# Performance work log

Measured on AMD Instinct MI355X. Metric: run time of the kernel, lower is better.

## Reference

```python
import jax, jax.numpy as jnp
import numpy as np

B, S, N, E = 8, 64, 512, 32  # batch, seq_size, node_num, embed_size


def setup_inputs() -> dict:
    key = jax.random.key(0)
    k0, k1, k2, k3, k4 = jax.random.split(key, 5)
    x = jax.random.normal(k0, (B, S, N), dtype=jnp.float32)
    # lin_w: Linear(2*S, E) -> weight (E, 2*S), bias (E,)
    W = jax.random.normal(k1, (E, 2 * S), dtype=jnp.float32) * (1.0 / np.sqrt(2 * S))
    b_w = jax.random.normal(k2, (E,), dtype=jnp.float32) * 0.01
    # lin_a: Linear(E, 1) -> weight (E,), bias scalar
    Wa = jax.random.normal(k3, (E,), dtype=jnp.float32) * (1.0 / np.sqrt(E))
    b_a = jax.random.normal(k4, (), dtype=jnp.float32) * 0.01
    return {"x": x, "W": W, "b_w": b_w, "Wa": Wa, "b_a": b_a}


def reference(x, W, b_w, Wa, b_a):
    # Faithful to MP_GAT.forward in eval mode (dropout = identity).
    # Algebraic decomposition: lin_w(cat(vi, vj)) = vi @ Wi^T + vj @ Wj^T + b,
    # where W = [Wi | Wj] along the input dim -- avoids the O(N^2 * 2S) concat.
    s = W.shape[1] // 2
    v = jnp.transpose(x, (0, 2, 1))          # (B, N, S)
    Wi, Wj = W[:, :s], W[:, s:]              # (E, S) each
    ti = jnp.einsum('bns,es->bne', v, Wi)    # (B, N, E)
    tj = jnp.einsum('bns,es->bne', v, Wj)    # (B, N, E)
    pre = ti[:, :, None, :] + tj[:, None, :, :] + b_w  # (B, N, N, E)
    xw = jnp.where(pre > 0, pre, 0.2 * pre)  # LeakyReLU(0.2)
    e = jnp.einsum('bije,e->bij', xw, Wa) + b_a        # (B, N, N) = lin_a(...).squeeze
    attention = jax.nn.softmax(e, axis=2)
    h = jax.nn.sigmoid(jnp.einsum('bij,bjs->bis', attention, v))  # (B, N, S)
    return jnp.transpose(h, (0, 2, 1)), attention      # (B, S, N), (B, N, N)
```

## Files before the change

### kernel.cpp

```cpp
#include <hip/hip_runtime.h>
#include <math.h>

#define BB 8
#define SS 64
#define NN 512
#define EE 32
#define IT 16

__device__ __forceinline__ unsigned short f2bf(float f) {
    union { float f; unsigned u; } v; v.f = f;
    unsigned r = v.u + 0x7fffu + ((v.u >> 16) & 1u);
    return (unsigned short)(r >> 16);
}
__device__ __forceinline__ float bflo(unsigned u) { return __uint_as_float(u << 16); }
__device__ __forceinline__ float bfhi(unsigned u) { return __uint_as_float(u & 0xffff0000u); }

__device__ __forceinline__ float qsum(float v) {
    v += __int_as_float(__builtin_amdgcn_mov_dpp(__float_as_int(v), 0xB1, 0xF, 0xF, true));
    v += __int_as_float(__builtin_amdgcn_mov_dpp(__float_as_int(v), 0x4E, 0xF, 0xF, true));
    return v;
}

__global__ __launch_bounds__(128) void proj_kernel(
    const float* __restrict__ x, const float* __restrict__ W,
    const float* __restrict__ b_w, const float* __restrict__ Wa,
    float* __restrict__ tip, unsigned short* __restrict__ tjb,
    float* __restrict__ cip, float* __restrict__ djp)
{
    __shared__ float sW[SS][65];
    const int t = threadIdx.x;
    const int wg = ((blockIdx.x & 7) << 6) | (blockIdx.x >> 3);
    const int b = wg >> 6;
    const int n0 = (wg & 63) << 3;

#pragma unroll
    for (int r = 0; r < 8; ++r) {
        int idx = r * 512 + t * 4;
        float4 w4 = *(const float4*)(W + idx);
        int e = idx >> 7;
        int sp = idx & 127;
        int eo = ((sp >> 6) << 5) | e;
        int s0 = sp & 63;
        sW[s0 + 0][eo] = w4.x;
        sW[s0 + 1][eo] = w4.y;
        sW[s0 + 2][eo] = w4.z;
        sW[s0 + 3][eo] = w4.w;
    }
    __syncthreads();

    const int eo = t & 63;
    const int ng = t >> 6;
    const float* xb = x + (size_t)b * SS * NN + n0 + (ng << 2);
    float a0 = 0.f, a1 = 0.f, a2 = 0.f, a3 = 0.f;
#pragma unroll 8
    for (int s = 0; s < SS; ++s) {
        float wv = sW[s][eo];
        float4 xv = *(const float4*)(xb + (size_t)s * NN);
        a0 = fmaf(wv, xv.x, a0);
        a1 = fmaf(wv, xv.y, a1);
        a2 = fmaf(wv, xv.z, a2);
        a3 = fmaf(wv, xv.w, a3);
    }
    const int e = eo & 31;
    const bool isI = eo < EE;
    if (isI) {
        float bias = b_w[e];
        a0 += bias; a1 += bias; a2 += bias; a3 += bias;
        *(float4*)(tip + ((size_t)(b * EE + e)) * NN + n0 + (ng << 2)) =
            make_float4(a0, a1, a2, a3);
    } else {
        unsigned u0 = f2bf(a0) | ((unsigned)f2bf(a1) << 16);
        unsigned u1 = f2bf(a2) | ((unsigned)f2bf(a3) << 16);
        *(uint2*)(tjb + ((size_t)(b * EE + e)) * NN + n0 + (ng << 2)) =
            make_uint2(u0, u1);
    }

    float wa = Wa[e];
    float r0 = wa * a0, r1 = wa * a1, r2 = wa * a2, r3 = wa * a3;
#pragma unroll
    for (int off = 1; off <= 16; off <<= 1) {
        r0 += __shfl_xor(r0, off);
        r1 += __shfl_xor(r1, off);
        r2 += __shfl_xor(r2, off);
        r3 += __shfl_xor(r3, off);
    }
    if (eo == 0)
        *(float4*)(cip + (size_t)b * NN + n0 + (ng << 2)) = make_float4(r0, r1, r2, r3);
    if (eo == 32)
        *(float4*)(djp + (size_t)b * NN + n0 + (ng << 2)) = make_float4(r0, r1, r2, r3);
}

__global__ __launch_bounds__(512, 2) void attn_kernel(
    const float* __restrict__ x,
    const float* __restrict__ tip,
    const unsigned short* __restrict__ tjb,
    const float* __restrict__ cip,
    const float* __restrict__ djp,
    const float* __restrict__ Wa,
    float* __restrict__ out0,
    float* __restrict__ out1)
{
    __shared__ __align__(16) unsigned short stj[EE * NN];
    __shared__ __align__(16) unsigned scT[NN * 12];
    __shared__ __align__(16) float s_tiT[IT][36];
    __shared__ __align__(16) float hp[8 * SS * 20];
    __shared__ __align__(16) float red[8][IT];
    __shared__ float s_inv[IT];

    const int t = threadIdx.x;
    const int wg = ((blockIdx.x & 7) << 5) | (blockIdx.x >> 3);
    const int b = wg >> 5;
    const int i0 = (wg & 31) << 4;
    const int lane = t & 63;
    const int w = t >> 6;

    {
        int i = t & 15, e = t >> 4;
        s_tiT[i][e] = tip[((size_t)(b * EE + e)) * NN + i0 + i];
    }
    {
        const uint4* src = (const uint4*)(tjb + (size_t)b * EE * NN);
        uint4* dst = (uint4*)stj;
#pragma unroll
        for (int r = 0; r < 4; ++r) dst[r * 512 + t] = src[r * 512 + t];
    }
    __syncthreads();

    const int ip = t & 7;
    const int jc = t >> 3;
    const int j0 = jc << 3;
    const int ia = 2 * ip, ib2 = 2 * ip + 1;

    float rti0[EE], rti1[EE];
#pragma unroll
    for (int q = 0; q < 8; ++q) {
        float4 v = *(const float4*)&s_tiT[ia][q << 2];
        rti0[4 * q + 0] = v.x; rti0[4 * q + 1] = v.y;
        rti0[4 * q + 2] = v.z; rti0[4 * q + 3] = v.w;
        float4 u = *(const float4*)&s_tiT[ib2][q << 2];
        rti1[4 * q + 0] = u.x; rti1[4 * q + 1] = u.y;
        rti1[4 * q + 2] = u.z; rti1[4 * q + 3] = u.w;
    }

    float acc0[8], acc1[8];
#pragma unroll
    for (int k = 0; k < 8; ++k) { acc0[k] = 0.f; acc1[k] = 0.f; }

#pragma unroll
    for (int e = 0; e < EE; ++e) {
        uint4 d = *(const uint4*)&stj[e * NN + j0];
        float wa = Wa[e];
        float t0 = rti0[e], t1 = rti1[e];
        float tjf[8];
        tjf[0] = bflo(d.x); tjf[1] = bfhi(d.x);
        tjf[2] = bflo(d.y); tjf[3] = bfhi(d.y);
        tjf[4] = bflo(d.z); tjf[5] = bfhi(d.z);
        tjf[6] = bflo(d.w); tjf[7] = bfhi(d.w);
#pragma unroll
        for (int k = 0; k < 8; ++k) {
            acc0[k] = fmaf(fabsf(t0 + tjf[k]), wa, acc0[k]);
            acc1[k] = fmaf(fabsf(t1 + tjf[k]), wa, acc1[k]);
        }
    }

    float dj8[8];
    {
        float4 d0 = *(const float4*)(djp + (size_t)b * NN + j0);
        float4 d1 = *(const float4*)(djp + (size_t)b * NN + j0 + 4);
        dj8[0] = d0.x; dj8[1] = d0.y; dj8[2] = d0.z; dj8[3] = d0.w;
        dj8[4] = d1.x; dj8[5] = d1.y; dj8[6] = d1.z; dj8[7] = d1.w;
    }
    float c0 = cip[(size_t)b * NN + i0 + ia];
    float c1 = cip[(size_t)b * NN + i0 + ib2];
    float pr0[8], pr1[8];
#pragma unroll
    for (int k = 0; k < 8; ++k) {
        pr0[k] = __expf(fmaf(0.4f, acc0[k], 0.6f * (c0 + dj8[k])));
        pr1[k] = __expf(fmaf(0.4f, acc1[k], 0.6f * (c1 + dj8[k])));
    }

#pragma unroll
    for (int k = 0; k < 8; ++k) {
        scT[(j0 + k) * 12 + ip] = f2bf(pr0[k]) | ((unsigned)f2bf(pr1[k]) << 16);
    }

    float rs0 = 0.f, rs1 = 0.f;
#pragma unroll
    for (int k = 0; k < 8; ++k) { rs0 += pr0[k]; rs1 += pr1[k]; }
#pragma unroll
    for (int off = 8; off <= 32; off <<= 1) {
        rs0 += __shfl_xor(rs0, off);
        rs1 += __shfl_xor(rs1, off);
    }
    if (lane < 8) { red[w][2 * lane] = rs0; red[w][2 * lane + 1] = rs1; }
    __syncthreads();
    if (t < IT) {
        float S = 0.f;
#pragma unroll
        for (int ww = 0; ww < 8; ++ww) S += red[ww][t];
        s_inv[t] = 1.0f / S;
    }
    __syncthreads();

    {
        float v0 = s_inv[ia], v1 = s_inv[ib2];
        float* r0p = out1 + ((size_t)(b * NN + i0 + ia)) * NN + j0;
        float* r1p = out1 + ((size_t)(b * NN + i0 + ib2)) * NN + j0;
        *(float4*)(r0p)     = make_float4(pr0[0]*v0, pr0[1]*v0, pr0[2]*v0, pr0[3]*v0);
        *(float4*)(r0p + 4) = make_float4(pr0[4]*v0, pr0[5]*v0, pr0[6]*v0, pr0[7]*v0);
        *(float4*)(r1p)     = make_float4(pr1[0]*v1, pr1[1]*v1, pr1[2]*v1, pr1[3]*v1);
        *(float4*)(r1p + 4) = make_float4(pr1[4]*v1, pr1[5]*v1, pr1[6]*v1, pr1[7]*v1);
    }

    const int jw = t & 3;
    const int sq = (t >> 2) & 7;
    const int ih = (t >> 5) & 1;
    const int w8 = t >> 6;
    float pacc[8][8];
#pragma unroll
    for (int r = 0; r < 8; ++r)
#pragma unroll
        for (int c = 0; c < 8; ++c) pacc[r][c] = 0.f;

    const float* xbb = x + (size_t)b * SS * NN;
#pragma unroll
    for (int uu = 0; uu < 4; ++uu) {
        const int jb = uu * 128 + w8 * 16 + jw * 4;
        float xq[8][4];
#pragma unroll
        for (int r = 0; r < 8; ++r) {
            float4 xv = *(const float4*)(xbb + (size_t)(sq + 8 * r) * NN + jb);
            xq[r][0] = xv.x; xq[r][1] = xv.y; xq[r][2] = xv.z; xq[r][3] = xv.w;
        }
#pragma unroll
        for (int v = 0; v < 4; ++v) {
            uint4 dd = *(const uint4*)&scT[(jb + v) * 12 + (ih << 2)];
            float ps[8];
            ps[0] = bflo(dd.x); ps[1] = bfhi(dd.x);
            ps[2] = bflo(dd.y); ps[3] = bfhi(dd.y);
            ps[4] = bflo(dd.z); ps[5] = bfhi(dd.z);
            ps[6] = bflo(dd.w); ps[7] = bfhi(dd.w);
#pragma unroll
            for (int r = 0; r < 8; ++r) {
                float xv = xq[r][v];
#pragma unroll
                for (int c = 0; c < 8; ++c)
                    pacc[r][c] = fmaf(xv, ps[c], pacc[r][c]);
            }
        }
    }

#pragma unroll
    for (int r = 0; r < 8; ++r)
#pragma unroll
        for (int c = 0; c < 8; ++c) pacc[r][c] = qsum(pacc[r][c]);

    if (jw == 0) {
#pragma unroll
        for (int r = 0; r < 8; ++r) {
            int s = sq + 8 * r;
            float* hq = &hp[(w8 * SS + s) * 20 + ih * 8];
            *(float4*)(hq)     = make_float4(pacc[r][0], pacc[r][1], pacc[r][2], pacc[r][3]);
            *(float4*)(hq + 4) = make_float4(pacc[r][4], pacc[r][5], pacc[r][6], pacc[r][7]);
        }
    }
    __syncthreads();

    {
        int i = t & 15, sb = t >> 4;
        float vi = s_inv[i];
#pragma unroll
        for (int rr = 0; rr < 2; ++rr) {
            int s = sb + 32 * rr;
            float h = 0.f;
#pragma unroll
            for (int ww = 0; ww < 8; ++ww) h += hp[(ww * SS + s) * 20 + i];
            h *= vi;
            out0[((size_t)(b * SS + s)) * NN + i0 + i] = 1.0f / (1.0f + __expf(-h));
        }
    }
}

extern "C" void kernel_launch(void* const* d_in, const int* in_sizes, int n_in,
                              void* d_out, int out_size, void* d_ws, size_t ws_size,
                              hipStream_t stream) {
    const float* x   = (const float*)d_in[0];
    const float* W   = (const float*)d_in[1];
    const float* b_w = (const float*)d_in[2];
    const float* Wa  = (const float*)d_in[3];

    float* out0 = (float*)d_out;
    float* out1 = (float*)d_out + (size_t)BB * SS * NN;

    float* tip = (float*)d_ws;
    unsigned short* tjb = (unsigned short*)(tip + (size_t)BB * EE * NN);
    float* cip = (float*)(tjb + (size_t)BB * EE * NN);
    float* djp = cip + (size_t)BB * NN;

    proj_kernel<<<BB * (NN / 8), 128, 0, stream>>>(x, W, b_w, Wa, tip, tjb, cip, djp);
    attn_kernel<<<BB * (NN / IT), 512, 0, stream>>>(x, tip, tjb, cip, djp, Wa, out0, out1);
}
```

Before: 22.22 us.

## Double attention block threads and read bf16 tj directly from global memory

The attention kernel now runs with 1024 threads per block instead of 512. Each thread scores 4 j columns instead of 8 and covers half as many j chunks in the attention-times-V loop, and the per-wave partial-sum buffers grow to 16 entries. The shared-memory staging of the bf16 tj tile is removed, so each thread loads tj straight from global memory. The aim is more parallelism and less LDS copying, but it costs heavier register pressure under the tighter launch bounds, a larger hp reduction buffer, and uncoalesced global reads of tj repeated across blocks.

```diff
diff --git a/kernel.cpp b/kernel.cpp
--- a/kernel.cpp
+++ b/kernel.cpp
@@ -90,7 +90,7 @@
         *(float4*)(djp + (size_t)b * NN + n0 + (ng << 2)) = make_float4(r0, r1, r2, r3);
 }
 
-__global__ __launch_bounds__(512, 2) void attn_kernel(
+__global__ __launch_bounds__(1024, 4) void attn_kernel(
     const float* __restrict__ x,
     const float* __restrict__ tip,
     const unsigned short* __restrict__ tjb,
@@ -100,11 +100,10 @@
     float* __restrict__ out0,
     float* __restrict__ out1)
 {
-    __shared__ __align__(16) unsigned short stj[EE * NN];
     __shared__ __align__(16) unsigned scT[NN * 12];
+    __shared__ __align__(16) float hp[16 * SS * 20];
     __shared__ __align__(16) float s_tiT[IT][36];
-    __shared__ __align__(16) float hp[8 * SS * 20];
-    __shared__ __align__(16) float red[8][IT];
+    __shared__ __align__(16) float red[16][IT];
     __shared__ float s_inv[IT];
 
     const int t = threadIdx.x;
@@ -112,23 +111,23 @@
     const int b = wg >> 5;
     const int i0 = (wg & 31) << 4;
     const int lane = t & 63;
-    const int w = t >> 6;
-
-    {
+    const int w16 = t >> 6;
+
+    if (t < 256) {
         int i = t & 15, e = t >> 4;
         s_tiT[i][e] = tip[((size_t)(b * EE + e)) * NN + i0 + i];
-    }
-    {
-        const uint4* src = (const uint4*)(tjb + (size_t)b * EE * NN);
-        uint4* dst = (uint4*)stj;
-#pragma unroll
-        for (int r = 0; r < 4; ++r) dst[r * 512 + t] = src[r * 512 + t];
+        if (t < IT * EE - 256) {}
+    }
+    if (t >= 256 && t < 512) {
+        int tt = t;
+        int i = tt & 15, e = tt >> 4;
+        s_tiT[i][e] = tip[((size_t)(b * EE + e)) * NN + i0 + i];
     }
     __syncthreads();
 
     const int ip = t & 7;
     const int jc = t >> 3;
-    const int j0 = jc << 3;
+    const int j0 = jc << 2;
     const int ia = 2 * ip, ib2 = 2 * ip + 1;
 
     float rti0[EE], rti1[EE];
@@ -142,80 +141,69 @@
         rti1[4 * q + 2] = u.z; rti1[4 * q + 3] = u.w;
     }
 
-    float acc0[8], acc1[8];
-#pragma unroll
-    for (int k = 0; k < 8; ++k) { acc0[k] = 0.f; acc1[k] = 0.f; }
-
+    float acc0[4], acc1[4];
+#pragma unroll
+    for (int k = 0; k < 4; ++k) { acc0[k] = 0.f; acc1[k] = 0.f; }
+
+    const unsigned short* tjbb = tjb + (size_t)b * EE * NN + j0;
 #pragma unroll
     for (int e = 0; e < EE; ++e) {
-        uint4 d = *(const uint4*)&stj[e * NN + j0];
+        uint2 d = *(const uint2*)(tjbb + (size_t)e * NN);
         float wa = Wa[e];
         float t0 = rti0[e], t1 = rti1[e];
-        float tjf[8];
+        float tjf[4];
         tjf[0] = bflo(d.x); tjf[1] = bfhi(d.x);
         tjf[2] = bflo(d.y); tjf[3] = bfhi(d.y);
-        tjf[4] = bflo(d.z); tjf[5] = bfhi(d.z);
-        tjf[6] = bflo(d.w); tjf[7] = bfhi(d.w);
-#pragma unroll
-        for (int k = 0; k < 8; ++k) {
+#pragma unroll
+        for (int k = 0; k < 4; ++k) {
             acc0[k] = fmaf(fabsf(t0 + tjf[k]), wa, acc0[k]);
             acc1[k] = fmaf(fabsf(t1 + tjf[k]), wa, acc1[k]);
         }
     }
 
-    float dj8[8];
-    {
-        float4 d0 = *(const float4*)(djp + (size_t)b * NN + j0);
-        float4 d1 = *(const float4*)(djp + (size_t)b * NN + j0 + 4);
-        dj8[0] = d0.x; dj8[1] = d0.y; dj8[2] = d0.z; dj8[3] = d0.w;
-        dj8[4] = d1.x; dj8[5] = d1.y; dj8[6] = d1.z; dj8[7] = d1.w;
-    }
+    float4 dj4 = *(const float4*)(djp + (size_t)b * NN + j0);
+    float dj[4] = {dj4.x, dj4.y, dj4.z, dj4.w};
     float c0 = cip[(size_t)b * NN + i0 + ia];
     float c1 = cip[(size_t)b * NN + i0 + ib2];
-    float pr0[8], pr1[8];
-#pragma unroll
-    for (int k = 0; k < 8; ++k) {
-        pr0[k] = __expf(fmaf(0.4f, acc0[k], 0.6f * (c0 + dj8[k])));
-        pr1[k] = __expf(fmaf(0.4f, acc1[k], 0.6f * (c1 + dj8[k])));
-    }
-
-#pragma unroll
-    for (int k = 0; k < 8; ++k) {
+    float pr0[4], pr1[4];
+#pragma unroll
+    for (int k = 0; k < 4; ++k) {
+        pr0[k] = __expf(fmaf(0.4f, acc0[k], 0.6f * (c0 + dj[k])));
+        pr1[k] = __expf(fmaf(0.4f, acc1[k], 0.6f * (c1 + dj[k])));
+    }
+
+#pragma unroll
+    for (int k = 0; k < 4; ++k)
         scT[(j0 + k) * 12 + ip] = f2bf(pr0[k]) | ((unsigned)f2bf(pr1[k]) << 16);
-    }
-
-    float rs0 = 0.f, rs1 = 0.f;
-#pragma unroll
-    for (int k = 0; k < 8; ++k) { rs0 += pr0[k]; rs1 += pr1[k]; }
+
+    float rs0 = pr0[0] + pr0[1] + pr0[2] + pr0[3];
+    float rs1 = pr1[0] + pr1[1] + pr1[2] + pr1[3];
 #pragma unroll
     for (int off = 8; off <= 32; off <<= 1) {
         rs0 += __shfl_xor(rs0, off);
         rs1 += __shfl_xor(rs1, off);
     }
-    if (lane < 8) { red[w][2 * lane] = rs0; red[w][2 * lane + 1] = rs1; }
+    if (lane < 8) { red[w16][2 * lane] = rs0; red[w16][2 * lane + 1] = rs1; }
     __syncthreads();
     if (t < IT) {
         float S = 0.f;
 #pragma unroll
-        for (int ww = 0; ww < 8; ++ww) S += red[ww][t];
+        for (int ww = 0; ww < 16; ++ww) S += red[ww][t];
         s_inv[t] = 1.0f / S;
     }
     __syncthreads();
 
     {
         float v0 = s_inv[ia], v1 = s_inv[ib2];
-        float* r0p = out1 + ((size_t)(b * NN + i0 + ia)) * NN + j0;
-        float* r1p = out1 + ((size_t)(b * NN + i0 + ib2)) * NN + j0;
-        *(float4*)(r0p)     = make_float4(pr0[0]*v0, pr0[1]*v0, pr0[2]*v0, pr0[3]*v0);
-        *(float4*)(r0p + 4) = make_float4(pr0[4]*v0, pr0[5]*v0, pr0[6]*v0, pr0[7]*v0);
-        *(float4*)(r1p)     = make_float4(pr1[0]*v1, pr1[1]*v1, pr1[2]*v1, pr1[3]*v1);
-        *(float4*)(r1p + 4) = make_float4(pr1[4]*v1, pr1[5]*v1, pr1[6]*v1, pr1[7]*v1);
+        *(float4*)(out1 + ((size_t)(b * NN + i0 + ia)) * NN + j0) =
+            make_float4(pr0[0]*v0, pr0[1]*v0, pr0[2]*v0, pr0[3]*v0);
+        *(float4*)(out1 + ((size_t)(b * NN + i0 + ib2)) * NN + j0) =
+            make_float4(pr1[0]*v1, pr1[1]*v1, pr1[2]*v1, pr1[3]*v1);
     }
 
     const int jw = t & 3;
     const int sq = (t >> 2) & 7;
     const int ih = (t >> 5) & 1;
-    const int w8 = t >> 6;
     float pacc[8][8];
 #pragma unroll
     for (int r = 0; r < 8; ++r)
@@ -224,8 +212,8 @@
 
     const float* xbb = x + (size_t)b * SS * NN;
 #pragma unroll
-    for (int uu = 0; uu < 4; ++uu) {
-        const int jb = uu * 128 + w8 * 16 + jw * 4;
+    for (int uu = 0; uu < 2; ++uu) {
+        const int jb = (w16 << 5) + (uu << 4) + (jw << 2);
         float xq[8][4];
 #pragma unroll
         for (int r = 0; r < 8; ++r) {
@@ -259,7 +247,7 @@
 #pragma unroll
         for (int r = 0; r < 8; ++r) {
             int s = sq + 8 * r;
-            float* hq = &hp[(w8 * SS + s) * 20 + ih * 8];
+            float* hq = &hp[(w16 * SS + s) * 20 + ih * 8];
             *(float4*)(hq)     = make_float4(pacc[r][0], pacc[r][1], pacc[r][2], pacc[r][3]);
             *(float4*)(hq + 4) = make_float4(pacc[r][4], pacc[r][5], pacc[r][6], pacc[r][7]);
         }
@@ -267,17 +255,12 @@
     __syncthreads();
 
     {
-        int i = t & 15, sb = t >> 4;
-        float vi = s_inv[i];
-#pragma unroll
-        for (int rr = 0; rr < 2; ++rr) {
-            int s = sb + 32 * rr;
-            float h = 0.f;
-#pragma unroll
-            for (int ww = 0; ww < 8; ++ww) h += hp[(ww * SS + s) * 20 + i];
-            h *= vi;
-            out0[((size_t)(b * SS + s)) * NN + i0 + i] = 1.0f / (1.0f + __expf(-h));
-        }
+        int i = t & 15, s = t >> 4;
+        float h = 0.f;
+#pragma unroll
+        for (int ww = 0; ww < 16; ++ww) h += hp[(ww * SS + s) * 20 + i];
+        h *= s_inv[i];
+        out0[((size_t)(b * SS + s)) * NN + i0 + i] = 1.0f / (1.0f + __expf(-h));
     }
 }
 
@@ -298,5 +281,5 @@
     float* djp = cip + (size_t)BB * NN;
 
     proj_kernel<<<BB * (NN / 8), 128, 0, stream>>>(x, W, b_w, Wa, tip, tjb, cip, djp);
-    attn_kernel<<<BB * (NN / IT), 512, 0, stream>>>(x, tip, tjb, cip, djp, Wa, out0, out1);
-}
+    attn_kernel<<<BB * (NN / IT), 1024, 0, stream>>>(x, tip, tjb, cip, djp, Wa, out0, out1);
+}
```

Result: slower. 32.54 us (+46.4%).

## Compute attention-weighted sum with bf16 MFMA instead of scalar FMAs

Applied to the files above, without the earlier changes.

Replaces the per-thread scalar FMA outer-product for h = P·x with __builtin_amdgcn_mfma_f32_16x16x32_bf16. The unnormalized probabilities are stored row-major as bf16 in LDS, and x is truncated to bf16 on the fly. This cuts VALU work and the DPP cross-lane reductions, and shrinks the partial-sum buffer from 8 warps to 2 K-halves. In exchange x loses precision through bf16 truncation without rounding, and the accumulation order changes.

```diff
diff --git a/kernel.cpp b/kernel.cpp
--- a/kernel.cpp
+++ b/kernel.cpp
@@ -7,6 +7,9 @@
 #define EE 32
 #define IT 16
 
+typedef __attribute__((ext_vector_type(8))) short short8v;
+typedef __attribute__((ext_vector_type(4))) float f32x4;
+
 __device__ __forceinline__ unsigned short f2bf(float f) {
     union { float f; unsigned u; } v; v.f = f;
     unsigned r = v.u + 0x7fffu + ((v.u >> 16) & 1u);
@@ -14,11 +17,8 @@
 }
 __device__ __forceinline__ float bflo(unsigned u) { return __uint_as_float(u << 16); }
 __device__ __forceinline__ float bfhi(unsigned u) { return __uint_as_float(u & 0xffff0000u); }
-
-__device__ __forceinline__ float qsum(float v) {
-    v += __int_as_float(__builtin_amdgcn_mov_dpp(__float_as_int(v), 0xB1, 0xF, 0xF, true));
-    v += __int_as_float(__builtin_amdgcn_mov_dpp(__float_as_int(v), 0x4E, 0xF, 0xF, true));
-    return v;
+__device__ __forceinline__ unsigned packtr(float lo, float hi) {
+    return (__float_as_uint(hi) & 0xffff0000u) | (__float_as_uint(lo) >> 16);
 }
 
 __global__ __launch_bounds__(128) void proj_kernel(
@@ -101,9 +101,9 @@
     float* __restrict__ out1)
 {
     __shared__ __align__(16) unsigned short stj[EE * NN];
-    __shared__ __align__(16) unsigned scT[NN * 12];
+    __shared__ __align__(16) unsigned short prT[IT * 520];
     __shared__ __align__(16) float s_tiT[IT][36];
-    __shared__ __align__(16) float hp[8 * SS * 20];
+    __shared__ __align__(16) float hp[2][SS][17];
     __shared__ __align__(16) float red[8][IT];
     __shared__ float s_inv[IT];
 
@@ -179,9 +179,18 @@
         pr1[k] = __expf(fmaf(0.4f, acc1[k], 0.6f * (c1 + dj8[k])));
     }
 
-#pragma unroll
-    for (int k = 0; k < 8; ++k) {
-        scT[(j0 + k) * 12 + ip] = f2bf(pr0[k]) | ((unsigned)f2bf(pr1[k]) << 16);
+    {
+        uint4 pa, pb;
+        pa.x = f2bf(pr0[0]) | ((unsigned)f2bf(pr0[1]) << 16);
+        pa.y = f2bf(pr0[2]) | ((unsigned)f2bf(pr0[3]) << 16);
+        pa.z = f2bf(pr0[4]) | ((unsigned)f2bf(pr0[5]) << 16);
+        pa.w = f2bf(pr0[6]) | ((unsigned)f2bf(pr0[7]) << 16);
+        pb.x = f2bf(pr1[0]) | ((unsigned)f2bf(pr1[1]) << 16);
+        pb.y = f2bf(pr1[2]) | ((unsigned)f2bf(pr1[3]) << 16);
+        pb.z = f2bf(pr1[4]) | ((unsigned)f2bf(pr1[5]) << 16);
+        pb.w = f2bf(pr1[6]) | ((unsigned)f2bf(pr1[7]) << 16);
+        *(uint4*)&prT[ia * 520 + j0]  = pa;
+        *(uint4*)&prT[ib2 * 520 + j0] = pb;
     }
 
     float rs0 = 0.f, rs1 = 0.f;
@@ -212,56 +221,31 @@
         *(float4*)(r1p + 4) = make_float4(pr1[4]*v1, pr1[5]*v1, pr1[6]*v1, pr1[7]*v1);
     }
 
-    const int jw = t & 3;
-    const int sq = (t >> 2) & 7;
-    const int ih = (t >> 5) & 1;
-    const int w8 = t >> 6;
-    float pacc[8][8];
-#pragma unroll
-    for (int r = 0; r < 8; ++r)
-#pragma unroll
-        for (int c = 0; c < 8; ++c) pacc[r][c] = 0.f;
-
-    const float* xbb = x + (size_t)b * SS * NN;
-#pragma unroll
-    for (int uu = 0; uu < 4; ++uu) {
-        const int jb = uu * 128 + w8 * 16 + jw * 4;
-        float xq[8][4];
-#pragma unroll
-        for (int r = 0; r < 8; ++r) {
-            float4 xv = *(const float4*)(xbb + (size_t)(sq + 8 * r) * NN + jb);
-            xq[r][0] = xv.x; xq[r][1] = xv.y; xq[r][2] = xv.z; xq[r][3] = xv.w;
-        }
-#pragma unroll
-        for (int v = 0; v < 4; ++v) {
-            uint4 dd = *(const uint4*)&scT[(jb + v) * 12 + (ih << 2)];
-            float ps[8];
-            ps[0] = bflo(dd.x); ps[1] = bfhi(dd.x);
-            ps[2] = bflo(dd.y); ps[3] = bfhi(dd.y);
-            ps[4] = bflo(dd.z); ps[5] = bfhi(dd.z);
-            ps[6] = bflo(dd.w); ps[7] = bfhi(dd.w);
-#pragma unroll
-            for (int r = 0; r < 8; ++r) {
-                float xv = xq[r][v];
-#pragma unroll
-                for (int c = 0; c < 8; ++c)
-                    pacc[r][c] = fmaf(xv, ps[c], pacc[r][c]);
-            }
-        }
-    }
-
-#pragma unroll
-    for (int r = 0; r < 8; ++r)
-#pragma unroll
-        for (int c = 0; c < 8; ++c) pacc[r][c] = qsum(pacc[r][c]);
-
-    if (jw == 0) {
-#pragma unroll
-        for (int r = 0; r < 8; ++r) {
-            int s = sq + 8 * r;
-            float* hq = &hp[(w8 * SS + s) * 20 + ih * 8];
-            *(float4*)(hq)     = make_float4(pacc[r][0], pacc[r][1], pacc[r][2], pacc[r][3]);
-            *(float4*)(hq + 4) = make_float4(pacc[r][4], pacc[r][5], pacc[r][6], pacc[r][7]);
+    {
+        const int mt = w & 3;
+        const int kh = w >> 2;
+        const int lm = lane & 15;
+        const int ko = lane >> 4;
+        const float* xrow = x + ((size_t)(b * SS + mt * 16 + lm)) * NN;
+
+        f32x4 acc = {0.f, 0.f, 0.f, 0.f};
+#pragma unroll
+        for (int st = 0; st < 8; ++st) {
+            const int j = kh * 256 + st * 32 + ko * 8;
+            float4 xa = *(const float4*)(xrow + j);
+            float4 xb2 = *(const float4*)(xrow + j + 4);
+            union { unsigned u[4]; short8v v; } af;
+            af.u[0] = packtr(xa.x, xa.y);
+            af.u[1] = packtr(xa.z, xa.w);
+            af.u[2] = packtr(xb2.x, xb2.y);
+            af.u[3] = packtr(xb2.z, xb2.w);
+            short8v bf = *(const short8v*)&prT[lm * 520 + j];
+            acc = __builtin_amdgcn_mfma_f32_16x16x32_bf16(af.v, bf, acc, 0, 0, 0);
+        }
+#pragma unroll
+        for (int r = 0; r < 4; ++r) {
+            int s = mt * 16 + (lane >> 4) * 4 + r;
+            hp[kh][s][lm] = acc[r];
         }
     }
     __syncthreads();
@@ -272,10 +256,7 @@
 #pragma unroll
         for (int rr = 0; rr < 2; ++rr) {
             int s = sb + 32 * rr;
-            float h = 0.f;
-#pragma unroll
-            for (int ww = 0; ww < 8; ++ww) h += hp[(ww * SS + s) * 20 + i];
-            h *= vi;
+            float h = (hp[0][s][i] + hp[1][s][i]) * vi;
             out0[((size_t)(b * SS + s)) * NN + i0 + i] = 1.0f / (1.0f + __expf(-h));
         }
     }
```

Measured after the change: 20.38 us. -8.3%, faster.
